# Optimization experiments

Hardware: AMD Instinct MI355X
Metric: run time of the kernel (lower is better)

The kernel has to match this reference:

```python
import jax, jax.numpy as jnp
import numpy as np
import math

D_MODEL = 1024
NUM_HEADS = 16
HEAD_DIM = D_MODEL // NUM_HEADS


def setup_inputs() -> dict:
    key = jax.random.key(0)
    ks = jax.random.split(key, 9)
    B, S = 2, 2048
    scale = 1.0 / math.sqrt(D_MODEL)
    x = jax.random.normal(ks[0], (B, S, D_MODEL), dtype=jnp.float32)
    # torch nn.Linear params: weight [out, in], bias [out]
    Wq = jax.random.normal(ks[1], (D_MODEL, D_MODEL), dtype=jnp.float32) * scale
    bq = jax.random.normal(ks[2], (D_MODEL,), dtype=jnp.float32) * scale
    Wk = jax.random.normal(ks[3], (D_MODEL, D_MODEL), dtype=jnp.float32) * scale
    bk = jax.random.normal(ks[4], (D_MODEL,), dtype=jnp.float32) * scale
    Wv = jax.random.normal(ks[5], (D_MODEL, D_MODEL), dtype=jnp.float32) * scale
    bv = jax.random.normal(ks[6], (D_MODEL,), dtype=jnp.float32) * scale
    Wo = jax.random.normal(ks[7], (D_MODEL, D_MODEL), dtype=jnp.float32) * scale
    bo = jax.random.normal(ks[8], (D_MODEL,), dtype=jnp.float32) * scale
    return {"x": x, "Wq": Wq, "bq": bq, "Wk": Wk, "bk": bk,
            "Wv": Wv, "bv": bv, "Wo": Wo, "bo": bo}


def reference(x, Wq, bq, Wk, bk, Wv, bv, Wo, bo):
    B, S, _ = x.shape
    H, Dh = NUM_HEADS, HEAD_DIM

    def proj(W, b):
        # torch Linear: x @ W.T + b -> [B,S,D] -> [B,H,S,Dh]
        y = jnp.einsum('bsd,ed->bse', x, W) + b
        return y.reshape(B, S, H, Dh).transpose(0, 2, 1, 3)

    Q = proj(Wq, bq)
    K = proj(Wk, bk)
    V = proj(Wv, bv)

    # scores [B,H,S,S], causal mask with -inf, then scale by 1/sqrt(head_dim)
    scores = jnp.einsum('bhqd,bhkd->bhqk', Q, K)
    causal = jnp.tril(jnp.ones((S, S), dtype=bool))
    scores = jnp.where(causal, scores, -jnp.inf)
    A = jax.nn.softmax(scores / math.sqrt(Dh), axis=-1)

    O = jnp.einsum('bhqk,bhkd->bhqd', A, V)  # [B,H,S,Dh]
    O = O.transpose(0, 2, 1, 3).reshape(B, S, H * Dh)
    return jnp.einsum('bsd,ed->bse', O, Wo) + bo
```

## Files before the change

### kernel.cpp

```cpp
#include <hip/hip_runtime.h>


typedef _Float16 f16x8 __attribute__((ext_vector_type(8)));
typedef _Float16 f16x4 __attribute__((ext_vector_type(4)));
typedef _Float16 f16x2 __attribute__((ext_vector_type(2)));
typedef float f32x4 __attribute__((ext_vector_type(4)));

#define S_  2048
#define DM  1024
#define NH  16
#define DH  64

__device__ __forceinline__ void gload_lds16(const void* g, void* s) {
  __builtin_amdgcn_global_load_lds(
      (const __attribute__((address_space(1))) void*)g,
      (__attribute__((address_space(3))) void*)s, 16, 0, 0);
}

__device__ __forceinline__ f16x2 pkrtz(float a, float b) {
  return __builtin_bit_cast(f16x2, __builtin_amdgcn_cvt_pkrtz(a, b));
}


__global__ void cvt_all_kernel(const float* __restrict__ x,
                               const float* __restrict__ w0,
                               const float* __restrict__ w1,
                               const float* __restrict__ w2,
                               const float* __restrict__ w3,
                               _Float16* __restrict__ xb,
                               _Float16* __restrict__ wb) {
  const int bid = blockIdx.x;
  const float* src;
  _Float16* dst;
  int idx;
  if (bid < 4096) {
    src = x; dst = xb; idx = bid * 256 + threadIdx.x;
  } else {
    const int j = bid - 4096;
    const int y = j >> 10;
    src = (y == 0) ? w0 : (y == 1) ? w1 : (y == 2) ? w2 : w3;
    dst = wb + (size_t)y * (DM * DM);
    idx = (j & 1023) * 256 + threadIdx.x;
  }
  const float4 v = ((const float4*)src)[idx];
  f16x4 h;
  h[0] = (_Float16)v.x; h[1] = (_Float16)v.y;
  h[2] = (_Float16)v.z; h[3] = (_Float16)v.w;
  ((f16x4*)dst)[idx] = h;
}


__global__ __launch_bounds__(256, 2) void gemm_qkv_kernel(
    const _Float16* __restrict__ xb, const _Float16* __restrict__ wb,
    const float* __restrict__ bq, const float* __restrict__ bk,
    const float* __restrict__ bv, _Float16* __restrict__ qkv)
{
  __shared__ _Float16 As[2][128 * 32];
  __shared__ _Float16 Ws[2][128 * 32];
  const int z = blockIdx.z;
  const _Float16* W = wb + (size_t)z * (DM * DM);
  const float* bias = (z == 0) ? bq : ((z == 1) ? bk : bv);
  _Float16* out = qkv + (size_t)z * 4194304;

  const f32x4 z4 = {0.f, 0.f, 0.f, 0.f};
  f32x4 acc[4][4];
#pragma unroll
  for (int mi = 0; mi < 4; ++mi)
#pragma unroll
    for (int ni = 0; ni < 4; ++ni) acc[mi][ni] = z4;

  const int m0 = blockIdx.y * 128, n0 = blockIdx.x * 128;
  const int t = threadIdx.x;
  const int w = t >> 6, l = t & 63;
  const int quad = l >> 4, ln = l & 15;
  const int wm = (w >> 1) << 6, wn = (w & 1) << 6;
  const int srow = l >> 2, scol = (l & 3) << 3;

  for (int k0 = 0; k0 < DM; k0 += 64) {
#pragma unroll
    for (int h = 0; h < 2; ++h)
#pragma unroll
      for (int i = 0; i < 2; ++i) {
        const int ra = w * 32 + i * 16;
        gload_lds16(&xb[(size_t)(m0 + ra + srow) * DM + k0 + h * 32 + scol],
                    &As[h][ra * 32]);
        gload_lds16(&W[(size_t)(n0 + ra + srow) * DM + k0 + h * 32 + scol],
                    &Ws[h][ra * 32]);
      }
    __syncthreads();

#pragma unroll
    for (int h = 0; h < 2; ++h) {
      f16x8 af[4], bf[4];
#pragma unroll
      for (int mi = 0; mi < 4; ++mi)
        af[mi] = *(const f16x8*)&As[h][(wm + mi * 16 + ln) * 32 + quad * 8];
#pragma unroll
      for (int ni = 0; ni < 4; ++ni)
        bf[ni] = *(const f16x8*)&Ws[h][(wn + ni * 16 + ln) * 32 + quad * 8];
#pragma unroll
      for (int mi = 0; mi < 4; ++mi)
#pragma unroll
        for (int ni = 0; ni < 4; ++ni)
          acc[mi][ni] = __builtin_amdgcn_mfma_f32_16x16x32_f16(
              af[mi], bf[ni], acc[mi][ni], 0, 0, 0);
    }
    __syncthreads();
  }

  const float scale = (z == 0) ? 0.18033688f : 1.0f;

#pragma unroll
  for (int ni = 0; ni < 4; ++ni) {
    const int c = n0 + wn + ni * 16 + ln;
    const float bias_c = bias[c];
    const int h = c >> 6, d = c & 63;
#pragma unroll
    for (int mi = 0; mi < 4; ++mi) {
      const int mb = m0 + wm + mi * 16 + quad * 4;
#pragma unroll
      for (int r = 0; r < 4; ++r) {
        const int mg = mb + r;
        const int b = mg >> 11, s = mg & 2047;
        const int bh = b * NH + h;
        const float v = (acc[mi][ni][r] + bias_c) * scale;
        size_t idx;
        if (z == 2)
          idx = (size_t)bh * 131072 + (s >> 5) * 2048 + (d >> 4) * 512 +
                ((s >> 3) & 3) * 128 + (d & 15) * 8 + (s & 7);
        else
          idx = (size_t)bh * 131072 + (s >> 4) * 1024 + (d >> 5) * 512 +
                ((d >> 3) & 3) * 128 + (s & 15) * 8 + (d & 7);
        out[idx] = (_Float16)v;
      }
    }
  }
}


__global__ __launch_bounds__(256, 2) void gemm_out_kernel(
    const _Float16* __restrict__ ob, const _Float16* __restrict__ wo,
    const float* __restrict__ bo, float* __restrict__ out)
{
  __shared__ _Float16 As[2][128 * 32];
  __shared__ _Float16 Ws[2][64 * 32];
  const f32x4 z4 = {0.f, 0.f, 0.f, 0.f};
  f32x4 acc[2][4];
#pragma unroll
  for (int mi = 0; mi < 2; ++mi)
#pragma unroll
    for (int ni = 0; ni < 4; ++ni) acc[mi][ni] = z4;

  const int m0 = blockIdx.y * 128, n0 = blockIdx.x * 64;
  const int t = threadIdx.x;
  const int w = t >> 6, l = t & 63;
  const int quad = l >> 4, ln = l & 15;
  const int srow = l >> 2, scol = (l & 3) << 3;

  for (int k0 = 0; k0 < DM; k0 += 64) {
#pragma unroll
    for (int h = 0; h < 2; ++h) {
#pragma unroll
      for (int i = 0; i < 2; ++i) {
        const int ra = w * 32 + i * 16;
        gload_lds16(&ob[(size_t)(m0 + ra + srow) * DM + k0 + h * 32 + scol],
                    &As[h][ra * 32]);
      }
      gload_lds16(&wo[(size_t)(n0 + w * 16 + srow) * DM + k0 + h * 32 + scol],
                  &Ws[h][w * 16 * 32]);
    }
    __syncthreads();

#pragma unroll
    for (int h = 0; h < 2; ++h) {
      f16x8 af[2], bf[4];
#pragma unroll
      for (int mi = 0; mi < 2; ++mi)
        af[mi] = *(const f16x8*)&As[h][(w * 32 + mi * 16 + ln) * 32 + quad * 8];
#pragma unroll
      for (int ni = 0; ni < 4; ++ni)
        bf[ni] = *(const f16x8*)&Ws[h][(ni * 16 + ln) * 32 + quad * 8];
#pragma unroll
      for (int mi = 0; mi < 2; ++mi)
#pragma unroll
        for (int ni = 0; ni < 4; ++ni)
          acc[mi][ni] = __builtin_amdgcn_mfma_f32_16x16x32_f16(
              af[mi], bf[ni], acc[mi][ni], 0, 0, 0);
    }
    __syncthreads();
  }

#pragma unroll
  for (int ni = 0; ni < 4; ++ni) {
    const int c = n0 + ni * 16 + ln;
    const float bias_c = bo[c];
#pragma unroll
    for (int mi = 0; mi < 2; ++mi) {
      const int mb = m0 + w * 32 + mi * 16 + quad * 4;
#pragma unroll
      for (int r = 0; r < 4; ++r)
        out[(size_t)(mb + r) * DM + c] = acc[mi][ni][r] + bias_c;
    }
  }
}


template <bool DIAG>
__device__ __forceinline__ void tile_lds(
    const _Float16* __restrict__ Kls, const _Float16* __restrict__ Vls,
    const f16x8 (&qf)[2], f32x4 (&oacc)[4], float& l_i,
    _Float16* Ps, int quad, int ln, int l, int hq)
{
  const f32x4 z4 = {0.f, 0.f, 0.f, 0.f};
  f16x8 kv[4];

#pragma unroll
  for (int ii = 0; ii < 4; ++ii)
    kv[ii] = *(const f16x8*)&Kls[ii * 512 + l * 8];

  f32x4 sacc[2];
  sacc[0] = z4; sacc[1] = z4;
#pragma unroll
  for (int ks = 0; ks < 2; ++ks)
#pragma unroll
    for (int mi = 0; mi < 2; ++mi)
      sacc[mi] = __builtin_amdgcn_mfma_f32_16x16x32_f16(
          kv[mi * 2 + ks], qf[ks], sacc[mi], 0, 0, 0);

#pragma unroll
  for (int ii = 0; ii < 4; ++ii)
    kv[ii] = *(const f16x8*)&Vls[ii * 512 + l * 8];

  float rs = 0.f;
#pragma unroll
  for (int mi = 0; mi < 2; ++mi) {
    float p[4];
#pragma unroll
    for (int r = 0; r < 4; ++r) {
      p[r] = __builtin_amdgcn_exp2f(sacc[mi][r]);
      if (DIAG && (mi * 16 + quad * 4 + r > hq + ln)) p[r] = 0.f;
      rs += p[r];
    }
    const f16x2 lo = pkrtz(p[0], p[1]);
    const f16x2 hi = pkrtz(p[2], p[3]);
    const f16x4 pk = __builtin_shufflevector(lo, hi, 0, 1, 2, 3);
    const int slot = ((mi * 4 + quad) + 2 * ln) & 15;
    *(f16x4*)&Ps[ln * 64 + slot * 4] = pk;
  }
  l_i += rs;

  const int slot2 = ((quad * 2) + 2 * ln) & 15;
  const f16x8 pb = *(const f16x8*)&Ps[ln * 64 + slot2 * 4];

#pragma unroll
  for (int di = 0; di < 4; ++di)
    oacc[di] = __builtin_amdgcn_mfma_f32_16x16x32_f16(
        kv[di], pb, oacc[di], 0, 0, 0);
}

__global__ __launch_bounds__(256, 6) void attn_kernel(
    const _Float16* __restrict__ QF, const _Float16* __restrict__ KF,
    const _Float16* __restrict__ VF, _Float16* __restrict__ Ob)
{
  __shared__ _Float16 KVs[2][2][2048];
  __shared__ _Float16 Ps[4 * 16 * 64];

  const int i = blockIdx.x;
  const int bh = i & 31;
  const int b  = 31 - (i >> 5);
  const int T  = 2 * b + 2;

  const int tid = threadIdx.x;
  const int w = tid >> 6, l = tid & 63;
  const int quad = l >> 4, ln = l & 15;
  const int hq = (w & 1) << 4;
  const int Dw = 2 * b + (w >> 1);

  const _Float16* qb_ = QF + (size_t)bh * 131072;
  const _Float16* kb_ = KF + (size_t)bh * 131072;
  const _Float16* vb_ = VF + (size_t)bh * 131072;
  _Float16* psw = Ps + w * 1024;
  const int bidx = bh >> 4, hh = bh & 15;

  f16x8 qf[2];
#pragma unroll
  for (int ks = 0; ks < 2; ++ks)
    qf[ks] = *(const f16x8*)
        (qb_ + (size_t)((4 * b + w) * 2 + ks) * 512 + l * 8);

  const f32x4 z4 = {0.f, 0.f, 0.f, 0.f};
  f32x4 oacc[4];
#pragma unroll
  for (int di = 0; di < 4; ++di) oacc[di] = z4;
  float l_i = 0.f;

  gload_lds16(&kb_[(size_t)w * 512 + l * 8], &KVs[0][0][w * 512]);
  gload_lds16(&vb_[(size_t)w * 512 + l * 8], &KVs[0][1][w * 512]);

  for (int t = 0; t < T; ++t) {
    const int cur = t & 1;
    if (t + 1 < T) {
      gload_lds16(&kb_[(size_t)(t + 1) * 2048 + w * 512 + l * 8],
                  &KVs[cur ^ 1][0][w * 512]);
      gload_lds16(&vb_[(size_t)(t + 1) * 2048 + w * 512 + l * 8],
                  &KVs[cur ^ 1][1][w * 512]);
      asm volatile("s_waitcnt vmcnt(2)" ::: "memory");
    } else {
      asm volatile("s_waitcnt vmcnt(0)" ::: "memory");
    }
    __builtin_amdgcn_s_barrier();
    __builtin_amdgcn_sched_barrier(0);
    if (t < Dw)
      tile_lds<false>(&KVs[cur][0][0], &KVs[cur][1][0], qf, oacc, l_i,
                      psw, quad, ln, l, hq);
    else if (t == Dw)
      tile_lds<true>(&KVs[cur][0][0], &KVs[cur][1][0], qf, oacc, l_i,
                     psw, quad, ln, l, hq);
    __builtin_amdgcn_sched_barrier(0);
    __builtin_amdgcn_s_barrier();
  }

  l_i += __shfl_xor(l_i, 16);
  l_i += __shfl_xor(l_i, 32);
  const float inv = 1.0f / l_i;

  const int q = b * 64 + w * 16 + ln;
  _Float16* orow = Ob + (size_t)(bidx * S_ + q) * DM + hh * DH + quad * 4;
#pragma unroll
  for (int di = 0; di < 4; ++di) {
    f16x4 o4;
#pragma unroll
    for (int r = 0; r < 4; ++r)
      o4[r] = (_Float16)(oacc[di][r] * inv);
    *(f16x4*)(orow + di * 16) = o4;
  }
}


extern "C" void kernel_launch(void* const* d_in, const int* in_sizes, int n_in,
                              void* d_out, int out_size, void* d_ws, size_t ws_size,
                              hipStream_t stream) {
  (void)in_sizes; (void)n_in; (void)out_size; (void)ws_size;
  const float* x  = (const float*)d_in[0];
  const float* Wq = (const float*)d_in[1];
  const float* bq = (const float*)d_in[2];
  const float* Wk = (const float*)d_in[3];
  const float* bk = (const float*)d_in[4];
  const float* Wv = (const float*)d_in[5];
  const float* bv = (const float*)d_in[6];
  const float* Wo = (const float*)d_in[7];
  const float* bo = (const float*)d_in[8];

  char* ws = (char*)d_ws;
  _Float16* xb  = (_Float16*)(ws);
  _Float16* wb  = (_Float16*)(ws + (8u << 20));
  _Float16* qkv = (_Float16*)(ws + (16u << 20));
  _Float16* ob  = (_Float16*)(ws + (40u << 20));

  cvt_all_kernel<<<dim3(8192), dim3(256), 0, stream>>>(x, Wq, Wk, Wv, Wo, xb, wb);
  gemm_qkv_kernel<<<dim3(8, 32, 3), dim3(256), 0, stream>>>(xb, wb, bq, bk, bv, qkv);
  attn_kernel<<<dim3(1024), dim3(256), 0, stream>>>(
      qkv, qkv + 4194304, qkv + 2 * 4194304, ob);
  gemm_out_kernel<<<dim3(16, 32), dim3(256), 0, stream>>>(
      ob, wb + (size_t)3 * DM * DM, bo, (float*)d_out);
}
```

Before: 186.3 us.

## Process two KV tiles per barrier-synchronized iteration in causal attention

```diff
diff --git a/kernel.cpp b/kernel.cpp
--- a/kernel.cpp
+++ b/kernel.cpp
@@ -205,7 +205,7 @@
 }
 
 
-template <bool DIAG>
+template <int MODE>
 __device__ __forceinline__ void tile_lds(
     const _Float16* __restrict__ Kls, const _Float16* __restrict__ Vls,
     const f16x8 (&qf)[2], f32x4 (&oacc)[4], float& l_i,
@@ -238,7 +238,7 @@
 #pragma unroll
     for (int r = 0; r < 4; ++r) {
       p[r] = __builtin_amdgcn_exp2f(sacc[mi][r]);
-      if (DIAG && (mi * 16 + quad * 4 + r > hq + ln)) p[r] = 0.f;
+      if (MODE == 1 && (mi * 16 + quad * 4 + r > hq + ln)) p[r] = 0.f;
       rs += p[r];
     }
     const f16x2 lo = pkrtz(p[0], p[1]);
@@ -258,28 +258,28 @@
         kv[di], pb, oacc[di], 0, 0, 0);
 }
 
-__global__ __launch_bounds__(256, 6) void attn_kernel(
+__global__ __launch_bounds__(256, 3) void attn_kernel(
     const _Float16* __restrict__ QF, const _Float16* __restrict__ KF,
     const _Float16* __restrict__ VF, _Float16* __restrict__ Ob)
 {
-  __shared__ _Float16 KVs[2][2][2048];
-  __shared__ _Float16 Ps[4 * 16 * 64];
+  __shared__ _Float16 KVs[2][2][4096];
+  __shared__ _Float16 Ps[4][2][1024];
 
   const int i = blockIdx.x;
   const int bh = i & 31;
   const int b  = 31 - (i >> 5);
-  const int T  = 2 * b + 2;
 
   const int tid = threadIdx.x;
   const int w = tid >> 6, l = tid & 63;
   const int quad = l >> 4, ln = l & 15;
   const int hq = (w & 1) << 4;
-  const int Dw = 2 * b + (w >> 1);
+  const int g  = w >> 1;
 
   const _Float16* qb_ = QF + (size_t)bh * 131072;
   const _Float16* kb_ = KF + (size_t)bh * 131072;
   const _Float16* vb_ = VF + (size_t)bh * 131072;
-  _Float16* psw = Ps + w * 1024;
+  _Float16* psA = &Ps[w][0][0];
+  _Float16* psB = &Ps[w][1][0];
   const int bidx = bh >> 4, hh = bh & 15;
 
   f16x8 qf[2];
@@ -294,28 +294,38 @@
   for (int di = 0; di < 4; ++di) oacc[di] = z4;
   float l_i = 0.f;
 
-  gload_lds16(&kb_[(size_t)w * 512 + l * 8], &KVs[0][0][w * 512]);
-  gload_lds16(&vb_[(size_t)w * 512 + l * 8], &KVs[0][1][w * 512]);
-
-  for (int t = 0; t < T; ++t) {
-    const int cur = t & 1;
-    if (t + 1 < T) {
-      gload_lds16(&kb_[(size_t)(t + 1) * 2048 + w * 512 + l * 8],
-                  &KVs[cur ^ 1][0][w * 512]);
-      gload_lds16(&vb_[(size_t)(t + 1) * 2048 + w * 512 + l * 8],
-                  &KVs[cur ^ 1][1][w * 512]);
-      asm volatile("s_waitcnt vmcnt(2)" ::: "memory");
+  gload_lds16(&kb_[(size_t)w * 512 + l * 8],        &KVs[0][0][w * 512]);
+  gload_lds16(&kb_[(size_t)(2048 + w * 512) + l * 8], &KVs[0][0][2048 + w * 512]);
+  gload_lds16(&vb_[(size_t)w * 512 + l * 8],        &KVs[0][1][w * 512]);
+  gload_lds16(&vb_[(size_t)(2048 + w * 512) + l * 8], &KVs[0][1][2048 + w * 512]);
+
+  for (int pr = 0; pr <= b; ++pr) {
+    const int cur = pr & 1;
+    if (pr < b) {
+      const size_t off = (size_t)(pr + 1) * 4096;
+      gload_lds16(&kb_[off + w * 512 + l * 8],        &KVs[cur ^ 1][0][w * 512]);
+      gload_lds16(&kb_[off + 2048 + w * 512 + l * 8], &KVs[cur ^ 1][0][2048 + w * 512]);
+      gload_lds16(&vb_[off + w * 512 + l * 8],        &KVs[cur ^ 1][1][w * 512]);
+      gload_lds16(&vb_[off + 2048 + w * 512 + l * 8], &KVs[cur ^ 1][1][2048 + w * 512]);
+      asm volatile("s_waitcnt vmcnt(4)" ::: "memory");
     } else {
       asm volatile("s_waitcnt vmcnt(0)" ::: "memory");
     }
     __builtin_amdgcn_s_barrier();
     __builtin_amdgcn_sched_barrier(0);
-    if (t < Dw)
-      tile_lds<false>(&KVs[cur][0][0], &KVs[cur][1][0], qf, oacc, l_i,
-                      psw, quad, ln, l, hq);
-    else if (t == Dw)
-      tile_lds<true>(&KVs[cur][0][0], &KVs[cur][1][0], qf, oacc, l_i,
-                     psw, quad, ln, l, hq);
+    const _Float16* K0 = &KVs[cur][0][0];
+    const _Float16* V0 = &KVs[cur][1][0];
+    if (pr < b) {
+      tile_lds<0>(K0,        V0,        qf, oacc, l_i, psA, quad, ln, l, hq);
+      tile_lds<0>(K0 + 2048, V0 + 2048, qf, oacc, l_i, psB, quad, ln, l, hq);
+    } else {
+      if (g) {
+        tile_lds<0>(K0,        V0,        qf, oacc, l_i, psA, quad, ln, l, hq);
+        tile_lds<1>(K0 + 2048, V0 + 2048, qf, oacc, l_i, psB, quad, ln, l, hq);
+      } else {
+        tile_lds<1>(K0,        V0,        qf, oacc, l_i, psA, quad, ln, l, hq);
+      }
+    }
     __builtin_amdgcn_sched_barrier(0);
     __builtin_amdgcn_s_barrier();
   }
```

After: 183.1 us. Within noise of the previous version (-1.7%).
